# Kernel tuning notes

Hardware: AMD Instinct MI355X
Metric: run time of the kernel (lower is better)

The kernel has to match this reference:

```python
import jax, jax.numpy as jnp
import numpy as np

B, S, D, H = 4, 2048, 1024, 16
HD = D // H

def setup_inputs() -> dict:
    key = jax.random.key(0)
    ks = jax.random.split(key, 5)
    scale = 1.0 / np.sqrt(D)
    x = jax.random.normal(ks[0], (B, S, D), dtype=jnp.float32)
    w_qkv = jax.random.normal(ks[1], (D, 3 * D), dtype=jnp.float32) * scale
    b_qkv = jax.random.normal(ks[2], (3 * D,), dtype=jnp.float32) * 0.01
    w_proj = jax.random.normal(ks[3], (D, D), dtype=jnp.float32) * scale
    b_proj = jax.random.normal(ks[4], (D,), dtype=jnp.float32) * 0.01
    return {"x": x, "w_qkv": w_qkv, "b_qkv": b_qkv, "w_proj": w_proj, "b_proj": b_proj}

def reference(x, w_qkv, b_qkv, w_proj, b_proj):
    b, s, d = x.shape
    qkv = x @ w_qkv + b_qkv                      # [B,S,3D]
    qkv = qkv.reshape(b, s, 3, H, HD)
    q, k, v = jnp.moveaxis(qkv, 2, 0)            # each [B,S,H,HD]
    q = q.transpose(0, 2, 1, 3)                  # [B,H,S,HD]
    k = k.transpose(0, 2, 1, 3)
    v = v.transpose(0, 2, 1, 3)
    scale = 1.0 / jnp.sqrt(jnp.asarray(HD, dtype=x.dtype))
    scores = jnp.einsum('bhqd,bhkd->bhqk', q, k) * scale
    attn = jax.nn.softmax(scores, axis=-1)
    out = jnp.einsum('bhqk,bhkd->bhqd', attn, v)  # [B,H,S,HD]
    out = out.transpose(0, 2, 1, 3).reshape(b, s, d)
    return out @ w_proj + b_proj
```

## Files before the change

kernel.cpp:

```cpp
#include <hip/hip_runtime.h>

#define B_  4
#define S_  2048
#define D_  1024
#define H_  16
#define HD_ 64
#define M_  (B_*S_)
#define QSCALE 0.1803368801111204f

typedef unsigned short u16;
typedef __bf16 bf16x8 __attribute__((ext_vector_type(8)));
typedef __bf16 bf16x2 __attribute__((ext_vector_type(2)));
typedef float  f32x4  __attribute__((ext_vector_type(4)));
typedef float  f32x16 __attribute__((ext_vector_type(16)));

__device__ __forceinline__ u16 f2bf(float f) {
  unsigned int u = __float_as_uint(f);
  u += 0x7fffu + ((u >> 16) & 1u);
  return (u16)(u >> 16);
}
__device__ __forceinline__ unsigned int packbf2(float lo, float hi) {
#if __has_builtin(__builtin_amdgcn_cvt_pk_bf16_f32)
  union { bf16x2 v; unsigned int u; } c;
  c.v = __builtin_amdgcn_cvt_pk_bf16_f32(lo, hi);
  return c.u;
#else
  return (unsigned int)f2bf(lo) | ((unsigned int)f2bf(hi) << 16);
#endif
}
__device__ __forceinline__ void gld16(const void* g, void* l) {
  __builtin_amdgcn_global_load_lds(
      (const __attribute__((address_space(1))) unsigned int*)g,
      (__attribute__((address_space(3))) unsigned int*)l, 16, 0, 0);
}
#define MFMA32(a,b,c) __builtin_amdgcn_mfma_f32_32x32x16_bf16(a,b,c,0,0,0)
#define MFMA16(a,b,c) __builtin_amdgcn_mfma_f32_16x16x32_bf16(a,b,c,0,0,0)

__device__ __forceinline__ size_t off16e(int r, int k) {
  return ((size_t)((r >> 7) * 32 + (k >> 5))) * 4096
       + (size_t)((r >> 4) & 7) * 512
       + (size_t)(((k >> 3) & 3) * 16 + (r & 15)) * 8 + (k & 7);
}
__device__ __forceinline__ size_t offA32(int bh, int s, int hd) {
  return ((size_t)(bh * 32 + (s >> 6)) * 8 + ((s >> 5) & 1) * 4 + (hd >> 4)) * 512
       + (size_t)(((hd >> 3) & 1) * 32 + (s & 31)) * 8 + (hd & 7);
}
__device__ __forceinline__ size_t offVT(int bh, int s, int hd) {
  return ((size_t)(bh * 32 + (s >> 6)) * 8 + (hd >> 5) * 4 + ((s >> 4) & 3)) * 512
       + (size_t)(((s >> 3) & 1) * 32 + (hd & 31)) * 8 + (s & 7);
}

__global__ void cvt_f32_bf16(const float* __restrict__ in, u16* __restrict__ out, int n4) {
  int i = blockIdx.x * 256 + threadIdx.x;
  if (i < n4) {
    float4 v = ((const float4*)in)[i];
    int m = i >> 8;
    int k = (i & 255) * 4;
    *(uint2*)&out[off16e(m, k)] = make_uint2(packbf2(v.x, v.y), packbf2(v.z, v.w));
  }
}

__global__ void transpose_w(const float* __restrict__ in, u16* __restrict__ out, int R, int C) {
  __shared__ float tile[32][33];
  int c0 = blockIdx.x * 32, r0 = blockIdx.y * 32;
  int tx = threadIdx.x, ty = threadIdx.y;
  #pragma unroll
  for (int i = 0; i < 4; i++)
    tile[ty + i*8][tx] = in[(size_t)(r0 + ty + i*8) * C + c0 + tx];
  __syncthreads();
  #pragma unroll
  for (int i = 0; i < 4; i++)
    out[off16e(c0 + ty + i*8, r0 + tx)] = f2bf(tile[tx][ty + i*8]);
}

__global__ __launch_bounds__(256,2) void gemm_qkv(
    const u16* __restrict__ X, const u16* __restrict__ WT,
    const float* __restrict__ bias,
    u16* __restrict__ qb, u16* __restrict__ kb, u16* __restrict__ vb)
{
  __shared__ u16 As[2*8*512];
  __shared__ u16 Bs[2*8*512];
  const int t = threadIdx.x, w = t >> 6, l = t & 63;
  const int m0 = blockIdx.y * 128, n0 = blockIdx.x * 128;
  const u16* Ab = X  + (size_t)(m0 >> 7) * 32 * 4096;
  const u16* Bb = WT + (size_t)(n0 >> 7) * 32 * 4096;

  #pragma unroll
  for (int f2 = 0; f2 < 2; f2++) {
    gld16(Ab + (w*2+f2)*512 + l*8, (char*)As + (w*2+f2)*1024);
    gld16(Bb + (w*2+f2)*512 + l*8, (char*)Bs + (w*2+f2)*1024);
  }
  f32x4 acc[4][4] = {};
  const int af = (w >> 1) * 4, bf = (w & 1) * 4;
  for (int it = 0; it < 32; it++) {
    __syncthreads();
    const int cur = (it & 1) * 4096;
    if (it < 31) {
      const int nb = ((it + 1) & 1) * 8;
      const size_t gs = (size_t)(it + 1) * 4096;
      #pragma unroll
      for (int f2 = 0; f2 < 2; f2++) {
        gld16(Ab + gs + (w*2+f2)*512 + l*8, (char*)As + (nb + w*2+f2)*1024);
        gld16(Bb + gs + (w*2+f2)*512 + l*8, (char*)Bs + (nb + w*2+f2)*1024);
      }
    }
    bf16x8 a[4], b[4];
    #pragma unroll
    for (int mt = 0; mt < 4; mt++) a[mt] = *(const bf16x8*)(As + cur + (af+mt)*512 + l*8);
    #pragma unroll
    for (int nt = 0; nt < 4; nt++) b[nt] = *(const bf16x8*)(Bs + cur + (bf+nt)*512 + l*8);
    #pragma unroll
    for (int mt = 0; mt < 4; mt++)
      #pragma unroll
      for (int nt = 0; nt < 4; nt++)
        acc[mt][nt] = MFMA16(a[mt], b[nt], acc[mt][nt]);
  }
  const int wm = (w >> 1) * 64, wn = (w & 1) * 64, lr = l & 15, quad = l >> 4;
  #pragma unroll
  for (int mt = 0; mt < 4; mt++)
  #pragma unroll
  for (int nt = 0; nt < 4; nt++) {
    int n = n0 + wn + nt * 16 + lr;
    float bia = bias[n];
    int which = n >> 10, hh = (n >> 6) & 15, hd = n & 63;
    #pragma unroll
    for (int r = 0; r < 4; r++) {
      int m = m0 + wm + mt * 16 + quad * 4 + r;
      float v = acc[mt][nt][r] + bia;
      int bb = m >> 11, s = m & 2047, bh = bb * 16 + hh;
      if (which == 0)      qb[offA32(bh, s, hd)] = f2bf(v * QSCALE);
      else if (which == 1) kb[offA32(bh, s, hd)] = f2bf(v);
      else                 vb[offVT(bh, s, hd)] = f2bf(v);
    }
  }
}

__global__ __launch_bounds__(256,2) void gemm_proj(
    const u16* __restrict__ X, const u16* __restrict__ WT,
    const float* __restrict__ bias, float* __restrict__ out)
{
  __shared__ u16 As[2*8*512];
  __shared__ u16 Bs[2*8*512];
  const int t = threadIdx.x, w = t >> 6, l = t & 63;
  const int m0 = blockIdx.y * 128, n0 = blockIdx.x * 128;
  const u16* Ab = X  + (size_t)(m0 >> 7) * 32 * 4096;
  const u16* Bb = WT + (size_t)(n0 >> 7) * 32 * 4096;

  #pragma unroll
  for (int f2 = 0; f2 < 2; f2++) {
    gld16(Ab + (w*2+f2)*512 + l*8, (char*)As + (w*2+f2)*1024);
    gld16(Bb + (w*2+f2)*512 + l*8, (char*)Bs + (w*2+f2)*1024);
  }
  f32x4 acc[4][4] = {};
  const int af = (w >> 1) * 4, bf = (w & 1) * 4;
  for (int it = 0; it < 32; it++) {
    __syncthreads();
    const int cur = (it & 1) * 4096;
    if (it < 31) {
      const int nb = ((it + 1) & 1) * 8;
      const size_t gs = (size_t)(it + 1) * 4096;
      #pragma unroll
      for (int f2 = 0; f2 < 2; f2++) {
        gld16(Ab + gs + (w*2+f2)*512 + l*8, (char*)As + (nb + w*2+f2)*1024);
        gld16(Bb + gs + (w*2+f2)*512 + l*8, (char*)Bs + (nb + w*2+f2)*1024);
      }
    }
    bf16x8 a[4], b[4];
    #pragma unroll
    for (int mt = 0; mt < 4; mt++) a[mt] = *(const bf16x8*)(As + cur + (af+mt)*512 + l*8);
    #pragma unroll
    for (int nt = 0; nt < 4; nt++) b[nt] = *(const bf16x8*)(Bs + cur + (bf+nt)*512 + l*8);
    #pragma unroll
    for (int mt = 0; mt < 4; mt++)
      #pragma unroll
      for (int nt = 0; nt < 4; nt++)
        acc[mt][nt] = MFMA16(a[mt], b[nt], acc[mt][nt]);
  }
  const int wm = (w >> 1) * 64, wn = (w & 1) * 64, lr = l & 15, quad = l >> 4;
  #pragma unroll
  for (int mt = 0; mt < 4; mt++)
  #pragma unroll
  for (int nt = 0; nt < 4; nt++) {
    int n = n0 + wn + nt * 16 + lr;
    float bia = bias[n];
    #pragma unroll
    for (int r = 0; r < 4; r++) {
      int m = m0 + wm + mt * 16 + quad * 4 + r;
      out[(size_t)m * D_ + n] = acc[mt][nt][r] + bia;
    }
  }
}

__global__ __launch_bounds__(128,2) void attn(
    const u16* __restrict__ qb, const u16* __restrict__ kb,
    const u16* __restrict__ vt, u16* __restrict__ ob)
{
  __shared__ u16 Kl[2*8*512];
  __shared__ u16 Vl[2*8*512];
  __shared__ float redL[2][64];
  const int t = threadIdx.x, w = t >> 6, l = t & 63, l31 = l & 31, h = l >> 5;
  const int bh = blockIdx.y, b = bh >> 4, hh = bh & 15;
  const int qt = blockIdx.x;
  const int s0 = qt * 128 + w * 64;
  const u16* qp = qb + (size_t)bh * 131072;
  const u16* kp = kb + (size_t)bh * 131072;
  const u16* vp = vt + (size_t)bh * 131072;

  bf16x8 qa[2][4];
  #pragma unroll
  for (int g = 0; g < 2; g++)
    #pragma unroll
    for (int kk = 0; kk < 4; kk++)
      qa[g][kk] = *(const bf16x8*)(qp + ((size_t)(qt*2 + w) * 8 + g*4 + kk) * 512 + l*8);

  f32x16 o[2][2] = {};
  float l_[2] = {0.f, 0.f};

  #pragma unroll
  for (int j = 0; j < 4; j++) {
    gld16(kp + (size_t)(w*4 + j) * 512 + l*8, (char*)Kl + (w*4 + j)*1024);
    gld16(vp + (size_t)(w*4 + j) * 512 + l*8, (char*)Vl + (w*4 + j)*1024);
  }

  for (int kt = 0; kt < 32; kt++) {
    __syncthreads();
    const int cur = (kt & 1) * 4096;
    if (kt < 31) {
      const int nb = ((kt + 1) & 1) * 8;
      const size_t gs = (size_t)(kt + 1) * 4096;
      #pragma unroll
      for (int j = 0; j < 4; j++) {
        gld16(kp + gs + (w*4 + j)*512 + l*8, (char*)Kl + (nb + w*4 + j)*1024);
        gld16(vp + gs + (w*4 + j)*512 + l*8, (char*)Vl + (nb + w*4 + j)*1024);
      }
    }

    f32x16 sf[2][2] = {};
    #pragma unroll
    for (int kk = 0; kk < 4; kk++) {
      bf16x8 ka0 = *(const bf16x8*)(Kl + cur + (0*4 + kk)*512 + l*8);
      bf16x8 ka1 = *(const bf16x8*)(Kl + cur + (1*4 + kk)*512 + l*8);
      sf[0][0] = MFMA32(ka0, qa[0][kk], sf[0][0]);
      sf[0][1] = MFMA32(ka0, qa[1][kk], sf[0][1]);
      sf[1][0] = MFMA32(ka1, qa[0][kk], sf[1][0]);
      sf[1][1] = MFMA32(ka1, qa[1][kk], sf[1][1]);
    }

    unsigned int pk[2][2][4][2];
    #pragma unroll
    for (int g = 0; g < 2; g++) {
      float sa = 0.f, sb = 0.f, sc = 0.f, sd = 0.f;
      #pragma unroll
      for (int mt = 0; mt < 2; mt++)
        #pragma unroll
        for (int e = 0; e < 4; e++) {
          float p0 = __builtin_amdgcn_exp2f(sf[mt][g][4*e+0]);
          float p1 = __builtin_amdgcn_exp2f(sf[mt][g][4*e+1]);
          float p2 = __builtin_amdgcn_exp2f(sf[mt][g][4*e+2]);
          float p3 = __builtin_amdgcn_exp2f(sf[mt][g][4*e+3]);
          sa += p0; sb += p1; sc += p2; sd += p3;
          pk[mt][g][e][0] = packbf2(p0, p1);
          pk[mt][g][e][1] = packbf2(p2, p3);
        }
      float s = (sa + sb) + (sc + sd);
      s += __shfl_xor(s, 32);
      l_[g] += s;
    }

    #pragma unroll
    for (int kk2 = 0; kk2 < 4; kk2++) {
      const int mt = kk2 >> 1, k1 = kk2 & 1;
      bf16x8 bv0 = *(const bf16x8*)(Vl + cur + (0*4 + kk2)*512 + l*8);
      bf16x8 bv1 = *(const bf16x8*)(Vl + cur + (1*4 + kk2)*512 + l*8);
      #pragma unroll
      for (int g = 0; g < 2; g++) {
        unsigned int s0_ = h ? pk[mt][g][2*k1][0] : pk[mt][g][2*k1+1][0];
        unsigned int s1_ = h ? pk[mt][g][2*k1][1] : pk[mt][g][2*k1+1][1];
        unsigned int r0 = (unsigned int)__shfl_xor((int)s0_, 32);
        unsigned int r1 = (unsigned int)__shfl_xor((int)s1_, 32);
        union { unsigned int u[4]; bf16x8 v; } pa;
        pa.u[0] = h ? r0 : pk[mt][g][2*k1][0];
        pa.u[1] = h ? r1 : pk[mt][g][2*k1][1];
        pa.u[2] = h ? pk[mt][g][2*k1+1][0] : r0;
        pa.u[3] = h ? pk[mt][g][2*k1+1][1] : r1;
        o[g][0] = MFMA32(pa.v, bv0, o[g][0]);
        o[g][1] = MFMA32(pa.v, bv1, o[g][1]);
      }
    }
  }

  #pragma unroll
  for (int g = 0; g < 2; g++) redL[w][g*32 + l31] = 1.f / l_[g];
  __syncthreads();
  #pragma unroll
  for (int g = 0; g < 2; g++)
    #pragma unroll
    for (int rb = 0; rb < 4; rb++) {
      f32x4 iv4 = *(const f32x4*)&redL[w][g*32 + 8*rb + 4*h];
      #pragma unroll
      for (int c = 0; c < 4; c++) {
        int r = rb*4 + c;
        int row = s0 + g*32 + c + 8*rb + 4*h;
        int m = b * S_ + row;
        int d0 = hh*64 + l31, d1 = hh*64 + 32 + l31;
        ob[off16e(m, d0)] = f2bf(o[g][0][r] * iv4[c]);
        ob[off16e(m, d1)] = f2bf(o[g][1][r] * iv4[c]);
      }
    }
}

extern "C" void kernel_launch(void* const* d_in, const int* in_sizes, int n_in,
                              void* d_out, int out_size, void* d_ws, size_t ws_size,
                              hipStream_t stream) {
  const float* x      = (const float*)d_in[0];
  const float* w_qkv  = (const float*)d_in[1];
  const float* b_qkv  = (const float*)d_in[2];
  const float* w_proj = (const float*)d_in[3];
  const float* b_proj = (const float*)d_in[4];
  float* out = (float*)d_out;

  char* ws = (char*)d_ws;
  u16* xbf    = (u16*)ws; ws += (size_t)M_ * D_ * 2;
  u16* wqkvT  = (u16*)ws; ws += (size_t)3 * D_ * D_ * 2;
  u16* wprojT = (u16*)ws; ws += (size_t)D_ * D_ * 2;
  u16* qbuf   = (u16*)ws; ws += (size_t)M_ * D_ * 2;
  u16* kbuf   = (u16*)ws; ws += (size_t)M_ * D_ * 2;
  u16* vtbuf  = (u16*)ws; ws += (size_t)M_ * D_ * 2;
  u16* aobuf  = (u16*)ws; ws += (size_t)M_ * D_ * 2;

  cvt_f32_bf16<<<(M_ * D_ / 4 + 255) / 256, 256, 0, stream>>>(x, xbf, M_ * D_ / 4);
  transpose_w<<<dim3(3 * D_ / 32, D_ / 32), dim3(32, 8), 0, stream>>>(w_qkv, wqkvT, D_, 3 * D_);
  transpose_w<<<dim3(D_ / 32, D_ / 32), dim3(32, 8), 0, stream>>>(w_proj, wprojT, D_, D_);
  gemm_qkv<<<dim3(3 * D_ / 128, M_ / 128), 256, 0, stream>>>(xbf, wqkvT, b_qkv, qbuf, kbuf, vtbuf);
  attn<<<dim3(S_ / 128, B_ * H_), 128, 0, stream>>>(qbuf, kbuf, vtbuf, aobuf);
  gemm_proj<<<dim3(D_ / 128, M_ / 128), 256, 0, stream>>>(aobuf, wprojT, b_proj, out);
}
```

Measured before the change: 317.2 us.

## Use per-wave private K/V LDS buffers with vmcnt-based pipelining and XCD grid swizzle

Each wave now streams the full K and V tiles into its own LDS region and synchronizes with explicit s_waitcnt vmcnt instead of block barriers. V loads are issued before the QK MFMAs and the next K tile is prefetched during softmax. The grid is flattened and remapped so each XCD processes contiguous heads, improving L2 reuse of K/V. The change doubles per-block K/V global traffic and relies on LDS reads completing before async overwrites.

```diff
diff --git a/kernel.cpp b/kernel.cpp
--- a/kernel.cpp
+++ b/kernel.cpp
@@ -33,6 +33,8 @@
       (const __attribute__((address_space(1))) unsigned int*)g,
       (__attribute__((address_space(3))) unsigned int*)l, 16, 0, 0);
 }
+#define WAIT_VM8() asm volatile("s_waitcnt vmcnt(8)" ::: "memory")
+#define WAIT_VM0() asm volatile("s_waitcnt vmcnt(0)" ::: "memory")
 #define MFMA32(a,b,c) __builtin_amdgcn_mfma_f32_32x32x16_bf16(a,b,c,0,0,0)
 #define MFMA16(a,b,c) __builtin_amdgcn_mfma_f32_16x16x32_bf16(a,b,c,0,0,0)
 
@@ -195,16 +197,19 @@
     const u16* __restrict__ qb, const u16* __restrict__ kb,
     const u16* __restrict__ vt, u16* __restrict__ ob)
 {
-  __shared__ u16 Kl[2*8*512];
-  __shared__ u16 Vl[2*8*512];
+  __shared__ u16 Kl[2][8*512];
+  __shared__ u16 Vl[2][8*512];
   __shared__ float redL[2][64];
   const int t = threadIdx.x, w = t >> 6, l = t & 63, l31 = l & 31, h = l >> 5;
-  const int bh = blockIdx.y, b = bh >> 4, hh = bh & 15;
-  const int qt = blockIdx.x;
+  const int i = blockIdx.x, xcd = i & 7, j = i >> 3;
+  const int bh = xcd * 8 + (j >> 4), qt = j & 15;
+  const int b = bh >> 4, hh = bh & 15;
   const int s0 = qt * 128 + w * 64;
   const u16* qp = qb + (size_t)bh * 131072;
   const u16* kp = kb + (size_t)bh * 131072;
   const u16* vp = vt + (size_t)bh * 131072;
+  u16* myK = &Kl[w][0];
+  u16* myV = &Vl[w][0];
 
   bf16x8 qa[2][4];
   #pragma unroll
@@ -217,33 +222,33 @@
   float l_[2] = {0.f, 0.f};
 
   #pragma unroll
-  for (int j = 0; j < 4; j++) {
-    gld16(kp + (size_t)(w*4 + j) * 512 + l*8, (char*)Kl + (w*4 + j)*1024);
-    gld16(vp + (size_t)(w*4 + j) * 512 + l*8, (char*)Vl + (w*4 + j)*1024);
-  }
+  for (int f = 0; f < 8; f++)
+    gld16(kp + (size_t)f * 512 + l*8, (char*)myK + f*1024);
 
   for (int kt = 0; kt < 32; kt++) {
-    __syncthreads();
-    const int cur = (kt & 1) * 4096;
-    if (kt < 31) {
-      const int nb = ((kt + 1) & 1) * 8;
-      const size_t gs = (size_t)(kt + 1) * 4096;
-      #pragma unroll
-      for (int j = 0; j < 4; j++) {
-        gld16(kp + gs + (w*4 + j)*512 + l*8, (char*)Kl + (nb + w*4 + j)*1024);
-        gld16(vp + gs + (w*4 + j)*512 + l*8, (char*)Vl + (nb + w*4 + j)*1024);
-      }
-    }
+    const size_t gs = (size_t)kt * 4096;
+    #pragma unroll
+    for (int f = 0; f < 8; f++)
+      gld16(vp + gs + f*512 + l*8, (char*)myV + f*1024);
+
+    WAIT_VM8();
 
     f32x16 sf[2][2] = {};
     #pragma unroll
     for (int kk = 0; kk < 4; kk++) {
-      bf16x8 ka0 = *(const bf16x8*)(Kl + cur + (0*4 + kk)*512 + l*8);
-      bf16x8 ka1 = *(const bf16x8*)(Kl + cur + (1*4 + kk)*512 + l*8);
+      bf16x8 ka0 = *(const bf16x8*)(myK + (0*4 + kk)*512 + l*8);
+      bf16x8 ka1 = *(const bf16x8*)(myK + (1*4 + kk)*512 + l*8);
       sf[0][0] = MFMA32(ka0, qa[0][kk], sf[0][0]);
       sf[0][1] = MFMA32(ka0, qa[1][kk], sf[0][1]);
       sf[1][0] = MFMA32(ka1, qa[0][kk], sf[1][0]);
       sf[1][1] = MFMA32(ka1, qa[1][kk], sf[1][1]);
+    }
+
+    if (kt < 31) {
+      const size_t gs2 = (size_t)(kt + 1) * 4096;
+      #pragma unroll
+      for (int f = 0; f < 8; f++)
+        gld16(kp + gs2 + f*512 + l*8, (char*)myK + f*1024);
     }
 
     unsigned int pk[2][2][4][2];
@@ -267,11 +272,14 @@
       l_[g] += s;
     }
 
+    if (kt < 31) { WAIT_VM8(); }
+    else         { WAIT_VM0(); }
+
     #pragma unroll
     for (int kk2 = 0; kk2 < 4; kk2++) {
       const int mt = kk2 >> 1, k1 = kk2 & 1;
-      bf16x8 bv0 = *(const bf16x8*)(Vl + cur + (0*4 + kk2)*512 + l*8);
-      bf16x8 bv1 = *(const bf16x8*)(Vl + cur + (1*4 + kk2)*512 + l*8);
+      bf16x8 bv0 = *(const bf16x8*)(myV + (0*4 + kk2)*512 + l*8);
+      bf16x8 bv1 = *(const bf16x8*)(myV + (1*4 + kk2)*512 + l*8);
       #pragma unroll
       for (int g = 0; g < 2; g++) {
         unsigned int s0_ = h ? pk[mt][g][2*k1][0] : pk[mt][g][2*k1+1][0];
@@ -332,6 +340,6 @@
   transpose_w<<<dim3(3 * D_ / 32, D_ / 32), dim3(32, 8), 0, stream>>>(w_qkv, wqkvT, D_, 3 * D_);
   transpose_w<<<dim3(D_ / 32, D_ / 32), dim3(32, 8), 0, stream>>>(w_proj, wprojT, D_, D_);
   gemm_qkv<<<dim3(3 * D_ / 128, M_ / 128), 256, 0, stream>>>(xbf, wqkvT, b_qkv, qbuf, kbuf, vtbuf);
-  attn<<<dim3(S_ / 128, B_ * H_), 128, 0, stream>>>(qbuf, kbuf, vtbuf, aobuf);
+  attn<<<1024, 128, 0, stream>>>(qbuf, kbuf, vtbuf, aobuf);
   gemm_proj<<<dim3(D_ / 128, M_ / 128), 256, 0, stream>>>(aobuf, wprojT, b_proj, out);
 }
```

Result: faster. 297.5 us (-6.2%).
